# Optimization experiments

Hardware: AMD Instinct MI355X
Metric: run time of the kernel (lower is better)

The kernel has to match this reference:

```python
import jax, jax.numpy as jnp
import numpy as np

EPS = 1e-5

def conv2d(x, w, b=None, groups=1):
    out = jax.lax.conv_general_dilated(x, w, (1, 1), 'SAME',
                                       feature_group_count=groups,
                                       dimension_numbers=('NCHW', 'OIHW', 'NCHW'))
    return out if b is None else out + b[None, :, None, None]

def bn(x, g, beta):
    # BatchNorm2d in training mode: batch stats over (N, H, W), biased variance
    m = x.mean((0, 2, 3), keepdims=True)
    v = x.var((0, 2, 3), keepdims=True)
    return g[None, :, None, None] * (x - m) * jax.lax.rsqrt(v + EPS) + beta[None, :, None, None]

def up2x_align_corners(x):
    # nn.Upsample(scale_factor=2, mode='bilinear', align_corners=True)
    B, C, H, W = x.shape
    Ho, Wo = 2 * H, 2 * W
    ys = jnp.arange(Ho, dtype=jnp.float32) * (H - 1) / (Ho - 1)
    xs = jnp.arange(Wo, dtype=jnp.float32) * (W - 1) / (Wo - 1)
    y0 = jnp.floor(ys).astype(jnp.int32)
    x0 = jnp.floor(xs).astype(jnp.int32)
    y1 = jnp.minimum(y0 + 1, H - 1)
    x1 = jnp.minimum(x0 + 1, W - 1)
    wy = (ys - y0.astype(jnp.float32))[:, None]  # (Ho,1)
    wx = (xs - x0.astype(jnp.float32))[None, :]  # (1,Wo)
    r0 = x[:, :, y0, :]  # (B,C,Ho,W)
    r1 = x[:, :, y1, :]
    v00 = r0[:, :, :, x0]; v01 = r0[:, :, :, x1]
    v10 = r1[:, :, :, x0]; v11 = r1[:, :, :, x1]
    top = v00 * (1 - wx) + v01 * wx
    bot = v10 * (1 - wx) + v11 * wx
    return top * (1 - wy) + bot * wy


def setup_inputs() -> dict:
    key = jax.random.key(0)
    ks = jax.random.split(key, 10)
    B, C, H, W = 2, 64, 64, 64   # C = in_channels // 2
    K = 16                        # k_dim = C // k_factor
    OUT = 64                      # out_channels
    s = 0.1
    x1 = jax.random.normal(ks[0], (B, C, H, W), dtype=jnp.float32)
    x1_ = jax.random.normal(ks[1], (B, C, 2 * H, 2 * W), dtype=jnp.float32)
    x2_ = jax.random.normal(ks[2], (B, C, 2 * H, 2 * W), dtype=jnp.float32)
    Wq = jax.random.normal(ks[3], (C, 1, 3, 3), dtype=jnp.float32) * s   # depthwise
    bq = jnp.zeros((C,), jnp.float32)
    Wk = jax.random.normal(ks[4], (K, C, 3, 3), dtype=jnp.float32) * s
    bk = jnp.zeros((K,), jnp.float32)
    Wv = jax.random.normal(ks[5], (K,), dtype=jnp.float32) * s           # 1x1 conv, in=1
    bv = jnp.zeros((K,), jnp.float32)
    W1 = jax.random.normal(ks[6], (OUT, 2 * C, 3, 3), dtype=jnp.float32) * s
    g1 = jnp.ones((OUT,), jnp.float32); b1 = jnp.zeros((OUT,), jnp.float32)
    W2 = jax.random.normal(ks[7], (OUT, OUT, 3, 3), dtype=jnp.float32) * s
    g2 = jnp.ones((OUT,), jnp.float32); b2 = jnp.zeros((OUT,), jnp.float32)
    return dict(x1=x1, x1_=x1_, x2_=x2_, Wq=Wq, bq=bq, Wk=Wk, bk=bk, Wv=Wv, bv=bv,
                W1=W1, g1=g1, b1=b1, W2=W2, g2=g2, b2=b2)


def reference(x1, x1_, x2_, Wq, bq, Wk, bk, Wv, bv, W1, g1, b1, W2, g2, b2):
    # x1_ is accepted by the original forward but never used
    B, C, H, W = x1.shape
    x1u = up2x_align_corners(x1)                     # (B,C,2H,2W)
    dY = x2_.shape[2] - x1u.shape[2]
    dX = x2_.shape[3] - x1u.shape[3]
    x1u = jnp.pad(x1u, ((0, 0), (0, 0), (dY // 2, dY - dY // 2), (dX // 2, dX - dX // 2)))
    # Gatev_4(x=x1u, y=x1u, z=x2_): head_dim=1 SDPA -> scale = 1
    Q = jax.nn.relu(conv2d(x1u, Wq, bq, groups=C))   # (B,C,H2,W2)
    Kf = jax.nn.relu(conv2d(x1u, Wk, bk))            # (B,K,H2,W2), shared over C
    scores = Q[:, :, None] * Kf[:, None]             # (B,C,K,H2,W2)
    attn = jax.nn.softmax(scores, axis=2)
    V = jax.nn.relu(x2_[:, :, None] * Wv[None, None, :, None, None]
                    + bv[None, None, :, None, None])  # (B,C,K,H2,W2)
    gate = (attn * V).sum(axis=2)                    # (B,C,H2,W2)
    # DoubleConv(in=2C, out=OUT): conv3x3(no bias)->BN->ReLU x2
    h = jnp.concatenate([gate, x1u], axis=1)
    h = jax.nn.relu(bn(conv2d(h, W1), g1, b1))
    h = jax.nn.relu(bn(conv2d(h, W2), g2, b2))
    o1, o2 = jnp.split(h, 2, axis=1)
    return (o1, o2)
```

## Files before the change

### kernel.cpp

```cpp
#include <hip/hip_runtime.h>

#define HW 16384
#define PADPIX 16900

typedef __attribute__((ext_vector_type(8))) short short8v;
typedef __attribute__((ext_vector_type(4))) float f32x4;

__device__ inline short bf16rne(float x) {
    unsigned u = __float_as_uint(x);
    unsigned r = (u + 0x7fffu + ((u >> 16) & 1u)) >> 16;
    return (short)r;
}
__device__ inline float bf16tof(short s) {
    return __uint_as_float(((unsigned)(unsigned short)s) << 16);
}

__device__ inline int border_pp(int j) {
    if (j < 130) return j;
    if (j < 260) return 129 * 130 + (j - 130);
    if (j < 388) return (j - 259) * 130;
    return (j - 387) * 130 + 129;
}

__global__ __launch_bounds__(256) void k1_kernel(
    const float* __restrict__ W1, const float* __restrict__ W2,
    const float* __restrict__ Wk,
    short* __restrict__ Wb1, short* __restrict__ Wb2, short* __restrict__ Wbk,
    short* __restrict__ hcatN, short* __restrict__ h1N,
    float* __restrict__ statsAcc)
{
    int bid = blockIdx.x;
    const int t = threadIdx.x;
    if (bid == 565) {
        statsAcc[t] = 0.f;
        return;
    }
    if (bid < 468) {
        const float* W; short* Wb; int CIN, COUT, idx;
        if (bid < 288)      { W = W1; Wb = Wb1; CIN = 128; COUT = 64; idx = bid * 256 + t; }
        else if (bid < 432) { W = W2; Wb = Wb2; CIN = 64;  COUT = 64; idx = (bid - 288) * 256 + t; }
        else                { W = Wk; Wb = Wbk; CIN = 64;  COUT = 16; idx = (bid - 432) * 256 + t; }
        int NOCT = COUT >> 4, NCH = CIN >> 5;
        int total = 9 * NCH * NOCT * 512;
        if (idx >= total) return;
        int j = idx & 7, l = (idx >> 3) & 63;
        int rest = idx >> 9;
        int oct = rest % NOCT; rest /= NOCT;
        int ch = rest % NCH;
        int tap = rest / NCH;
        int o = oct * 16 + (l & 15);
        int c = ch * 32 + (l >> 4) * 8 + j;
        Wb[idx] = bf16rne(W[((size_t)o * CIN + c) * 9 + tap]);
        return;
    }
    int t2 = (bid - 468) * 256 + t;
    const int4 z = make_int4(0, 0, 0, 0);
    if (t2 < 16512) {
        int px = t2 >> 4, q = t2 & 15;
        int b = px >= 516; int j = px - b * 516;
        int pp = border_pp(j);
        ((int4*)hcatN)[((size_t)b * PADPIX + pp) * 16 + q] = z;
    } else if (t2 < 24768) {
        int idx = t2 - 16512;
        int px = idx >> 3, q = idx & 7;
        int b = px >= 516; int j = px - b * 516;
        int pp = border_pp(j);
        ((int4*)h1N)[((size_t)b * PADPIX + pp) * 8 + q] = z;
    }
}

#define UPSTR 72
#define UPROW (34 * UPSTR)
__global__ __launch_bounds__(256) void front_kernel(
    const float* __restrict__ x1, const short* __restrict__ Wbk,
    const float* __restrict__ bk, const float* __restrict__ Wq,
    const float* __restrict__ bq, const float* __restrict__ x2,
    const float* __restrict__ Wv, const float* __restrict__ bv,
    short* __restrict__ hcatN)
{
    __shared__ __align__(16) short upB[3 * UPROW];
    __shared__ float kfs[16 * 33];
    __shared__ float qbuf[32 * 65];
    __shared__ int tr[32 * 33];
    int bid = blockIdx.x;
    const int xq = bid & 3;
    const int y = (bid >> 2) & 127;
    const int b = bid >> 9;
    const int t = threadIdx.x;
    const int X0 = xq * 32;

    {
        const int px1 = t & 31, cg1 = t >> 5;
        const int gx = X0 + px1;
        float fx = (float)(gx * 63) / 127.f;
        int x0 = (int)fx; float wx = fx - (float)x0; int x1i = min(x0 + 1, 63);
        #pragma unroll
        for (int r = 0; r < 3; r++) {
            int ry = y + r - 1;
            bool rv = ((unsigned)ry < 128u);
            int ryc = rv ? ry : 0;
            float fy = (float)(ryc * 63) / 127.f;
            int y0 = (int)fy; float wy = fy - (float)y0; int y1 = min(y0 + 1, 63);
            int pk[4];
            #pragma unroll
            for (int jj = 0; jj < 4; jj++) {
                unsigned lohi[2];
                #pragma unroll
                for (int h = 0; h < 2; h++) {
                    int ch = cg1 * 8 + jj * 2 + h;
                    float v = 0.f;
                    if (rv) {
                        const float* sp = x1 + ((size_t)(b * 64 + ch) << 12);
                        float v00 = sp[(y0 << 6) + x0], v01 = sp[(y0 << 6) + x1i];
                        float v10 = sp[(y1 << 6) + x0], v11 = sp[(y1 << 6) + x1i];
                        float top = v00 * (1.f - wx) + v01 * wx;
                        float bot = v10 * (1.f - wx) + v11 * wx;
                        v = top * (1.f - wy) + bot * wy;
                    }
                    lohi[h] = (unsigned)(unsigned short)bf16rne(v);
                }
                pk[jj] = (int)(lohi[0] | (lohi[1] << 16));
            }
            *(int4*)(upB + r * UPROW + (px1 + 1) * UPSTR + cg1 * 8) =
                make_int4(pk[0], pk[1], pk[2], pk[3]);
        }
        if (t < 48) {
            int r = t >> 4, side = (t >> 3) & 1, cg = t & 7;
            int gxh = X0 + (side ? 32 : -1);
            int lpx = side ? 33 : 0;
            int ry = y + r - 1;
            bool v_ok = ((unsigned)ry < 128u) && ((unsigned)gxh < 128u);
            int ryc = ((unsigned)ry < 128u) ? ry : 0;
            float fy = (float)(ryc * 63) / 127.f;
            int y0 = (int)fy; float wy = fy - (float)y0; int y1 = min(y0 + 1, 63);
            int gxc = min(max(gxh, 0), 127);
            float fxh = (float)(gxc * 63) / 127.f;
            int hx0 = (int)fxh; float hwx = fxh - (float)hx0; int hx1 = min(hx0 + 1, 63);
            int pk[4];
            #pragma unroll
            for (int jj = 0; jj < 4; jj++) {
                unsigned lohi[2];
                #pragma unroll
                for (int h = 0; h < 2; h++) {
                    int ch = cg * 8 + jj * 2 + h;
                    float v = 0.f;
                    if (v_ok) {
                        const float* sp = x1 + ((size_t)(b * 64 + ch) << 12);
                        float v00 = sp[(y0 << 6) + hx0], v01 = sp[(y0 << 6) + hx1];
                        float v10 = sp[(y1 << 6) + hx0], v11 = sp[(y1 << 6) + hx1];
                        float top = v00 * (1.f - hwx) + v01 * hwx;
                        float bot = v10 * (1.f - hwx) + v11 * hwx;
                        v = top * (1.f - wy) + bot * wy;
                    }
                    lohi[h] = (unsigned)(unsigned short)bf16rne(v);
                }
                pk[jj] = (int)(lohi[0] | (lohi[1] << 16));
            }
            *(int4*)(upB + r * UPROW + lpx * UPSTR + cg * 8) =
                make_int4(pk[0], pk[1], pk[2], pk[3]);
        }
    }
    __syncthreads();

    {
        const int w = t >> 6, l = t & 63;
        if (w < 2) {
            const int lx = l & 15, kg = l >> 4;
            const short* wbase = Wbk + (size_t)l * 8;
            f32x4 acc = (f32x4)(0.f);
            #pragma unroll
            for (int ty = 0; ty < 3; ty++) {
                #pragma unroll
                for (int tx = 0; tx < 3; tx++) {
                    const short* ab = upB + ty * UPROW + (size_t)(w * 16 + lx + tx) * UPSTR;
                    #pragma unroll
                    for (int ch = 0; ch < 2; ch++) {
                        short8v a = *(const short8v*)(ab + kg * 8 + ch * 32);
                        short8v bf = *(const short8v*)(wbase +
                            (size_t)((ty * 3 + tx) * 2 + ch) * 512);
                        acc = __builtin_amdgcn_mfma_f32_16x16x32_bf16(a, bf, acc, 0, 0, 0);
                    }
                }
            }
            float bb = bk[lx];
            #pragma unroll
            for (int r = 0; r < 4; r++)
                kfs[lx * 33 + (w * 16 + kg * 4 + r)] = fmaxf(acc[r] + bb, 0.f);
        } else {
            const int ch = l;
            const int px0 = (w - 2) * 16;
            const float* wqp = Wq + ch * 9;
            float wq[9];
            #pragma unroll
            for (int i = 0; i < 9; i++) wq[i] = wqp[i];
            float bqc = bq[ch];
            float a0[3], a1[3];
            #pragma unroll
            for (int r = 0; r < 3; r++) {
                a0[r] = bf16tof(upB[r * UPROW + px0 * UPSTR + ch]);
                a1[r] = bf16tof(upB[r * UPROW + (px0 + 1) * UPSTR + ch]);
            }
            for (int p = 0; p < 16; p++) {
                float a2[3];
                #pragma unroll
                for (int r = 0; r < 3; r++)
                    a2[r] = bf16tof(upB[r * UPROW + (px0 + p + 2) * UPSTR + ch]);
                float q = bqc;
                #pragma unroll
                for (int r = 0; r < 3; r++)
                    q = fmaf(a0[r], wq[r * 3 + 0],
                        fmaf(a1[r], wq[r * 3 + 1], fmaf(a2[r], wq[r * 3 + 2], q)));
                qbuf[(px0 + p) * 65 + ch] = fmaxf(q, 0.f);
                #pragma unroll
                for (int r = 0; r < 3; r++) { a0[r] = a1[r]; a1[r] = a2[r]; }
            }
        }
    }
    __syncthreads();

    {
        const int px = t & 31, cg = t >> 5;
        const int x = X0 + px;
        float kv[16];
        #pragma unroll
        for (int k = 0; k < 16; k++) kv[k] = kfs[k * 33 + px];
        float kvmax = kv[0];
        #pragma unroll
        for (int k = 1; k < 16; k++) kvmax = fmaxf(kvmax, kv[k]);
        float wvv[16], bvv[16];
        #pragma unroll
        for (int k = 0; k < 16; k++) { wvv[k] = Wv[k]; bvv[k] = bv[k]; }
        float xvv[8], qv[8];
        #pragma unroll
        for (int j = 0; j < 8; j++) {
            xvv[j] = x2[((size_t)(b * 64 + cg * 8 + j) << 14) + (y << 7) + x];
            qv[j] = qbuf[px * 65 + cg * 8 + j];
        }
        #pragma unroll
        for (int jj = 0; jj < 4; jj++) {
            int gpk = 0;
            #pragma unroll
            for (int h = 0; h < 2; h++) {
                const int j = jj * 2 + h;
                float q = qv[j];
                float mx = q * kvmax;
                float den = 0.f, num = 0.f;
                #pragma unroll
                for (int k = 0; k < 16; k++) {
                    float e = __expf(fmaf(q, kv[k], -mx));
                    den += e;
                    float V = fmaxf(fmaf(xvv[j], wvv[k], bvv[k]), 0.f);
                    num = fmaf(e, V, num);
                }
                unsigned u = (unsigned)(unsigned short)bf16rne(num / den);
                gpk |= (int)(u << (h * 16));
            }
            tr[(cg * 4 + jj) * 33 + px] = gpk;
        }
    }
    __syncthreads();

    {
        const int px4 = t >> 3, cq = t & 7;
        int pp = (y + 1) * 130 + X0 + px4 + 1;
        int wd[4];
        #pragma unroll
        for (int i = 0; i < 4; i++) wd[i] = tr[(cq * 4 + i) * 33 + px4];
        int* dpL = (int*)hcatN + ((size_t)b * PADPIX + pp) * 64 + cq * 4;
        *(int4*)dpL = make_int4(wd[0], wd[1], wd[2], wd[3]);
        const short* us = upB + UPROW + (size_t)(px4 + 1) * UPSTR + cq * 8;
        int4 u = *(const int4*)us;
        int* dpU = (int*)hcatN + ((size_t)b * PADPIX + pp) * 64 + 32 + cq * 4;
        *(int4*)dpU = u;
    }
}

template<int PSTR, int LDSTR, int CIN, int COUT, int NWN, int OPW>
__global__ __launch_bounds__(256) void convmfma_kernel(
    const short* __restrict__ actN, const short* __restrict__ Wb,
    float* __restrict__ dst, float* __restrict__ partials)
{
    constexpr int NCH = CIN / 32, NOCT = COUT / 16, NWM = 4 / NWN;
    constexpr int EXT = NWM * 16;
    constexpr int SEG = 128 / EXT;
    __shared__ __align__(16) short slab[3 * 34 * LDSTR];
    const int t = threadIdx.x;
    const int w = t >> 6, l = t & 63;
    const int wn = w % NWN, wm = w / NWN;
    int bid = blockIdx.x;
    const int xseg = bid % SEG; bid /= SEG;
    const int y = bid & 127;
    const int b = bid >> 7;
    const int lx = l & 15, kg = l >> 4;
    const int X0 = xseg * EXT;

    constexpr int ROWI4 = 34 * PSTR / 8;
    constexpr int PXI4 = PSTR / 8;
    #pragma unroll
    for (int r = 0; r < 3; r++) {
        const int4* src = (const int4*)(actN +
            ((size_t)b * PADPIX + (size_t)(y + r) * 130 + X0) * PSTR);
        for (int i = t; i < ROWI4; i += 256) {
            int p = i / PXI4, cq = i % PXI4;
            *(int4*)(slab + (r * 34 + p) * LDSTR + cq * 8) = src[i];
        }
    }
    __syncthreads();

    const short* wbase = Wb + (size_t)(wn * OPW) * 512 + (size_t)l * 8;

    f32x4 acc[OPW];
    #pragma unroll
    for (int p = 0; p < OPW; p++) acc[p] = (f32x4)(0.f);

    #pragma unroll
    for (int ty = 0; ty < 3; ty++) {
        #pragma unroll
        for (int tx = 0; tx < 3; tx++) {
            const short* ab = slab + (ty * 34 + wm * 16 + lx + tx) * LDSTR + kg * 8;
            const int tap = ty * 3 + tx;
            #pragma unroll
            for (int ch = 0; ch < NCH; ch++) {
                short8v a = *(const short8v*)(ab + ch * 32);
                #pragma unroll
                for (int p = 0; p < OPW; p++) {
                    short8v bf = *(const short8v*)(wbase +
                        (size_t)((tap * NCH + ch) * NOCT + p) * 512);
                    acc[p] = __builtin_amdgcn_mfma_f32_16x16x32_bf16(a, bf, acc[p], 0, 0, 0);
                }
            }
        }
    }

    const int ox = X0 + wm * 16 + kg * 4;
    #pragma unroll
    for (int p = 0; p < OPW; p++) {
        const int oc = (wn * OPW + p) * 16 + lx;
        *(f32x4*)(dst + (((size_t)(b * COUT + oc)) << 14) + (y << 7) + ox) = acc[p];
    }

    #pragma unroll
    for (int p = 0; p < OPW; p++) {
        float s = 0.f, q2 = 0.f;
        f32x4 v = acc[p];
        #pragma unroll
        for (int r = 0; r < 4; r++) { s += v[r]; q2 = fmaf(v[r], v[r], q2); }
        s += __shfl_xor(s, 16); q2 += __shfl_xor(q2, 16);
        s += __shfl_xor(s, 32); q2 += __shfl_xor(q2, 32);
        if (l < 16) {
            const int oc = (wn * OPW + p) * 16 + lx;
            float* dp = partials + (((size_t)blockIdx.x * NWM + wm) * 64 + oc) * 2;
            dp[0] = s;
            dp[1] = q2;
        }
    }
}

__global__ void bnred_kernel(const float* __restrict__ partials,
                             float* __restrict__ statsAcc) {
    int ch = blockIdx.x;
    const int t = threadIdx.x;
    float s = 0.f, q = 0.f;
    for (int i = t; i < 2048; i += 256) {
        const float* p = partials + ((size_t)i * 64 + ch) * 2;
        s += p[0];
        q += p[1];
    }
    __shared__ float sh[512];
    sh[t] = s;
    sh[256 + t] = q;
    __syncthreads();
    for (int off = 128; off > 0; off >>= 1) {
        if (t < off) {
            sh[t] += sh[t + off];
            sh[256 + t] += sh[256 + t + off];
        }
        __syncthreads();
    }
    if (t == 0) {
        statsAcc[ch * 2] = sh[0];
        statsAcc[ch * 2 + 1] = sh[256];
    }
}

__global__ __launch_bounds__(256) void packN_kernel(
    const float* __restrict__ src, const float* __restrict__ statsAcc,
    const float* __restrict__ g, const float* __restrict__ beta,
    short* __restrict__ h1N)
{
    __shared__ int lds[32 * 65];
    int bid = blockIdx.x;
    const int pxt = bid & 255;
    const int b = bid >> 8;
    const int t = threadIdx.x;
    {
        const int cw = t >> 3, pg = t & 7;
        #pragma unroll
        for (int h = 0; h < 2; h++) {
            int c = cw * 2 + h;
            float mean = statsAcc[c * 2] * (1.f / 32768.f);
            float var  = statsAcc[c * 2 + 1] * (1.f / 32768.f) - mean * mean;
            float sc = g[c] * rsqrtf(var + 1e-5f);
            float sh = beta[c] - mean * sc;
            const float* sp = src + ((size_t)(b * 64 + c) << 14) + pxt * 64 + pg * 8;
            float4 v0 = *(const float4*)sp;
            float4 v1 = *(const float4*)(sp + 4);
            float vals[8] = {v0.x, v0.y, v0.z, v0.w, v1.x, v1.y, v1.z, v1.w};
            #pragma unroll
            for (int i = 0; i < 8; i++) {
                float v = fmaxf(fmaf(vals[i], sc, sh), 0.f);
                unsigned wv = (unsigned)(unsigned short)bf16rne(v);
                if (h == 0) lds[cw * 65 + pg * 8 + i] = (int)wv;
                else        lds[cw * 65 + pg * 8 + i] |= (int)(wv << 16);
            }
        }
    }
    __syncthreads();
    {
        const int px = t >> 2, cq = t & 3;
        int wd[8];
        #pragma unroll
        for (int i = 0; i < 8; i++) wd[i] = lds[(cq * 8 + i) * 65 + px];
        int pixel = pxt * 64 + px;
        int yy = pixel >> 7, xx = pixel & 127;
        int pp = (yy + 1) * 130 + xx + 1;
        int* dp = (int*)h1N + ((size_t)b * PADPIX + pp) * 32 + cq * 8;
        *(int4*)dp = make_int4(wd[0], wd[1], wd[2], wd[3]);
        *(int4*)(dp + 4) = make_int4(wd[4], wd[5], wd[6], wd[7]);
    }
}

__global__ void norm2_kernel(const float4* __restrict__ src,
                             const float* __restrict__ statsAcc,
                             const float* __restrict__ g, const float* __restrict__ beta,
                             float4* __restrict__ out) {
    int idx4 = blockIdx.x * 256 + threadIdx.x;
    int q = idx4 & 4095;
    int c = (idx4 >> 12) & 63;
    int b = idx4 >> 18;
    float mean = statsAcc[c * 2] * (1.f / 32768.f);
    float var  = statsAcc[c * 2 + 1] * (1.f / 32768.f) - mean * mean;
    float sc = g[c] * rsqrtf(var + 1e-5f);
    float sh = beta[c] - mean * sc;
    float4 v = src[idx4];
    v.x = fmaxf(fmaf(v.x, sc, sh), 0.f);
    v.y = fmaxf(fmaf(v.y, sc, sh), 0.f);
    v.z = fmaxf(fmaf(v.z, sc, sh), 0.f);
    v.w = fmaxf(fmaf(v.w, sc, sh), 0.f);
    int half = c >> 5, cc = c & 31;
    out[(size_t)half * 262144 + (((size_t)(b * 32 + cc)) << 12) + q] = v;
}

extern "C" void kernel_launch(void* const* d_in, const int* in_sizes, int n_in,
                              void* d_out, int out_size, void* d_ws, size_t ws_size,
                              hipStream_t stream) {
    const float* x1 = (const float*)d_in[0];
    const float* x2 = (const float*)d_in[2];
    const float* Wq = (const float*)d_in[3];
    const float* bq = (const float*)d_in[4];
    const float* Wk = (const float*)d_in[5];
    const float* bk = (const float*)d_in[6];
    const float* Wv = (const float*)d_in[7];
    const float* bv = (const float*)d_in[8];
    const float* W1 = (const float*)d_in[9];
    const float* g1 = (const float*)d_in[10];
    const float* b1 = (const float*)d_in[11];
    const float* W2 = (const float*)d_in[12];
    const float* g2 = (const float*)d_in[13];
    const float* b2 = (const float*)d_in[14];
    float* out = (float*)d_out;
    float* ws = (float*)d_ws;

    float* c1out    = ws;
    float* stacc    = ws + 2097152;
    short* hcatN    = (short*)(ws + 2097408);
    short* h1N      = (short*)(ws + 4260608);
    short* Wb1      = (short*)(ws + 5342208);
    short* Wb2      = (short*)(ws + 5379072);
    short* Wbk      = (short*)(ws + 5397504);
    float* partials = ws + 5402112;

    k1_kernel<<<566, 256, 0, stream>>>(W1, W2, Wk, Wb1, Wb2, Wbk, hcatN, h1N, stacc);

    front_kernel<<<1024, 256, 0, stream>>>(x1, Wbk, bk, Wq, bq, x2, Wv, bv, hcatN);

    convmfma_kernel<128, 136, 128, 64, 2, 2><<<1024, 256, 0, stream>>>(
        hcatN, Wb1, c1out, partials);
    bnred_kernel<<<64, 256, 0, stream>>>(partials, stacc);
    packN_kernel<<<512, 256, 0, stream>>>(c1out, stacc, g1, b1, h1N);

    convmfma_kernel<64, 72, 64, 64, 2, 2><<<1024, 256, 0, stream>>>(
        h1N, Wb2, c1out, partials);
    bnred_kernel<<<64, 256, 0, stream>>>(partials, stacc + 128);
    norm2_kernel<<<2048, 256, 0, stream>>>((const float4*)c1out, stacc + 128, g2, b2,
                                           (float4*)out);
}
```

Baseline: 75.71 us.

## Fuse BN1+ReLU into conv2 input load and emit bf16 conv1 output

```diff
diff --git a/kernel.cpp b/kernel.cpp
--- a/kernel.cpp
+++ b/kernel.cpp
@@ -26,15 +26,10 @@
     const float* __restrict__ W1, const float* __restrict__ W2,
     const float* __restrict__ Wk,
     short* __restrict__ Wb1, short* __restrict__ Wb2, short* __restrict__ Wbk,
-    short* __restrict__ hcatN, short* __restrict__ h1N,
-    float* __restrict__ statsAcc)
+    short* __restrict__ hcatN, short* __restrict__ h1N)
 {
     int bid = blockIdx.x;
     const int t = threadIdx.x;
-    if (bid == 565) {
-        statsAcc[t] = 0.f;
-        return;
-    }
     if (bid < 468) {
         const float* W; short* Wb; int CIN, COUT, idx;
         if (bid < 288)      { W = W1; Wb = Wb1; CIN = 128; COUT = 64; idx = bid * 256 + t; }
@@ -275,15 +270,20 @@
     }
 }
 
-template<int PSTR, int LDSTR, int CIN, int COUT, int NWN, int OPW>
+template<int PSTR, int LDSTR, int CIN, int COUT, int NWN, int OPW,
+         bool OUTBF16, bool INBN>
 __global__ __launch_bounds__(256) void convmfma_kernel(
     const short* __restrict__ actN, const short* __restrict__ Wb,
-    float* __restrict__ dst, float* __restrict__ partials)
+    float* __restrict__ dstF, short* __restrict__ dstB,
+    const float* __restrict__ statsAcc,
+    const float* __restrict__ g, const float* __restrict__ beta,
+    float* __restrict__ partials)
 {
     constexpr int NCH = CIN / 32, NOCT = COUT / 16, NWM = 4 / NWN;
     constexpr int EXT = NWM * 16;
     constexpr int SEG = 128 / EXT;
     __shared__ __align__(16) short slab[3 * 34 * LDSTR];
+    __shared__ float scsh[INBN ? 128 : 2];
     const int t = threadIdx.x;
     const int w = t >> 6, l = t & 63;
     const int wn = w % NWN, wm = w / NWN;
@@ -294,15 +294,49 @@
     const int lx = l & 15, kg = l >> 4;
     const int X0 = xseg * EXT;
 
+    if (INBN) {
+        if (t < 64) {
+            float mean = statsAcc[t * 2] * (1.f / 32768.f);
+            float var  = statsAcc[t * 2 + 1] * (1.f / 32768.f) - mean * mean;
+            float sc = g[t] * rsqrtf(var + 1e-5f);
+            scsh[t] = sc;
+            scsh[64 + t] = beta[t] - mean * sc;
+        }
+        __syncthreads();
+    }
+
     constexpr int ROWI4 = 34 * PSTR / 8;
     constexpr int PXI4 = PSTR / 8;
     #pragma unroll
     for (int r = 0; r < 3; r++) {
+        const int prow = y + r;
+        const bool rowb = (prow == 0) || (prow == 129);
         const int4* src = (const int4*)(actN +
-            ((size_t)b * PADPIX + (size_t)(y + r) * 130 + X0) * PSTR);
+            ((size_t)b * PADPIX + (size_t)prow * 130 + X0) * PSTR);
         for (int i = t; i < ROWI4; i += 256) {
             int p = i / PXI4, cq = i % PXI4;
-            *(int4*)(slab + (r * 34 + p) * LDSTR + cq * 8) = src[i];
+            int4 v = src[i];
+            if (INBN) {
+                int pcol = X0 + p;
+                if (rowb || pcol == 0 || pcol == 129) {
+                    v = make_int4(0, 0, 0, 0);
+                } else {
+                    int ch0 = cq * 8;
+                    int* vw = (int*)&v;
+                    #pragma unroll
+                    for (int wd = 0; wd < 4; wd++) {
+                        int c0 = ch0 + wd * 2, c1 = c0 + 1;
+                        float lo = bf16tof((short)(vw[wd] & 0xFFFF));
+                        float hi = bf16tof((short)((unsigned)vw[wd] >> 16));
+                        lo = fmaxf(fmaf(lo, scsh[c0], scsh[64 + c0]), 0.f);
+                        hi = fmaxf(fmaf(hi, scsh[c1], scsh[64 + c1]), 0.f);
+                        unsigned ulo = (unsigned)(unsigned short)bf16rne(lo);
+                        unsigned uhi = (unsigned)(unsigned short)bf16rne(hi);
+                        vw[wd] = (int)(ulo | (uhi << 16));
+                    }
+                }
+            }
+            *(int4*)(slab + (r * 34 + p) * LDSTR + cq * 8) = v;
         }
     }
     __syncthreads();
@@ -332,11 +366,24 @@
         }
     }
 
-    const int ox = X0 + wm * 16 + kg * 4;
-    #pragma unroll
-    for (int p = 0; p < OPW; p++) {
-        const int oc = (wn * OPW + p) * 16 + lx;
-        *(f32x4*)(dst + (((size_t)(b * COUT + oc)) << 14) + (y << 7) + ox) = acc[p];
+    if (OUTBF16) {
+        #pragma unroll
+        for (int p = 0; p < OPW; p++) {
+            const int oc = (wn * OPW + p) * 16 + lx;
+            #pragma unroll
+            for (int r = 0; r < 4; r++) {
+                const int px_x = X0 + wm * 16 + kg * 4 + r;
+                dstB[((size_t)b * PADPIX + (size_t)(y + 1) * 130 + px_x + 1) * 64 + oc] =
+                    bf16rne(acc[p][r]);
+            }
+        }
+    } else {
+        const int ox = X0 + wm * 16 + kg * 4;
+        #pragma unroll
+        for (int p = 0; p < OPW; p++) {
+            const int oc = (wn * OPW + p) * 16 + lx;
+            *(f32x4*)(dstF + (((size_t)(b * COUT + oc)) << 14) + (y << 7) + ox) = acc[p];
+        }
     }
 
     #pragma unroll
@@ -380,53 +427,6 @@
     if (t == 0) {
         statsAcc[ch * 2] = sh[0];
         statsAcc[ch * 2 + 1] = sh[256];
-    }
-}
-
-__global__ __launch_bounds__(256) void packN_kernel(
-    const float* __restrict__ src, const float* __restrict__ statsAcc,
-    const float* __restrict__ g, const float* __restrict__ beta,
-    short* __restrict__ h1N)
-{
-    __shared__ int lds[32 * 65];
-    int bid = blockIdx.x;
-    const int pxt = bid & 255;
-    const int b = bid >> 8;
-    const int t = threadIdx.x;
-    {
-        const int cw = t >> 3, pg = t & 7;
-        #pragma unroll
-        for (int h = 0; h < 2; h++) {
-            int c = cw * 2 + h;
-            float mean = statsAcc[c * 2] * (1.f / 32768.f);
-            float var  = statsAcc[c * 2 + 1] * (1.f / 32768.f) - mean * mean;
-            float sc = g[c] * rsqrtf(var + 1e-5f);
-            float sh = beta[c] - mean * sc;
-            const float* sp = src + ((size_t)(b * 64 + c) << 14) + pxt * 64 + pg * 8;
-            float4 v0 = *(const float4*)sp;
-            float4 v1 = *(const float4*)(sp + 4);
-            float vals[8] = {v0.x, v0.y, v0.z, v0.w, v1.x, v1.y, v1.z, v1.w};
-            #pragma unroll
-            for (int i = 0; i < 8; i++) {
-                float v = fmaxf(fmaf(vals[i], sc, sh), 0.f);
-                unsigned wv = (unsigned)(unsigned short)bf16rne(v);
-                if (h == 0) lds[cw * 65 + pg * 8 + i] = (int)wv;
-                else        lds[cw * 65 + pg * 8 + i] |= (int)(wv << 16);
-            }
-        }
-    }
-    __syncthreads();
-    {
-        const int px = t >> 2, cq = t & 3;
-        int wd[8];
-        #pragma unroll
-        for (int i = 0; i < 8; i++) wd[i] = lds[(cq * 8 + i) * 65 + px];
-        int pixel = pxt * 64 + px;
-        int yy = pixel >> 7, xx = pixel & 127;
-        int pp = (yy + 1) * 130 + xx + 1;
-        int* dp = (int*)h1N + ((size_t)b * PADPIX + pp) * 32 + cq * 8;
-        *(int4*)dp = make_int4(wd[0], wd[1], wd[2], wd[3]);
-        *(int4*)(dp + 4) = make_int4(wd[4], wd[5], wd[6], wd[7]);
     }
 }
 
@@ -480,18 +480,18 @@
     short* Wbk      = (short*)(ws + 5397504);
     float* partials = ws + 5402112;
 
-    k1_kernel<<<566, 256, 0, stream>>>(W1, W2, Wk, Wb1, Wb2, Wbk, hcatN, h1N, stacc);
+    k1_kernel<<<565, 256, 0, stream>>>(W1, W2, Wk, Wb1, Wb2, Wbk, hcatN, h1N);
 
     front_kernel<<<1024, 256, 0, stream>>>(x1, Wbk, bk, Wq, bq, x2, Wv, bv, hcatN);
 
-    convmfma_kernel<128, 136, 128, 64, 2, 2><<<1024, 256, 0, stream>>>(
-        hcatN, Wb1, c1out, partials);
+    convmfma_kernel<128, 136, 128, 64, 2, 2, true, false><<<1024, 256, 0, stream>>>(
+        hcatN, Wb1, nullptr, h1N, nullptr, nullptr, nullptr, partials);
     bnred_kernel<<<64, 256, 0, stream>>>(partials, stacc);
-    packN_kernel<<<512, 256, 0, stream>>>(c1out, stacc, g1, b1, h1N);
-
-    convmfma_kernel<64, 72, 64, 64, 2, 2><<<1024, 256, 0, stream>>>(
-        h1N, Wb2, c1out, partials);
+
+    convmfma_kernel<64, 72, 64, 64, 2, 2, false, true><<<1024, 256, 0, stream>>>(
+        h1N, Wb2, c1out, nullptr, stacc, g1, b1, partials);
     bnred_kernel<<<64, 256, 0, stream>>>(partials, stacc + 128);
+
     norm2_kernel<<<2048, 256, 0, stream>>>((const float4*)c1out, stacc + 128, g2, b2,
                                            (float4*)out);
 }
```

Result: faster. 70.12 us (-7.4%).
